# Kernel optimization log

Hardware: AMD Instinct MI355X
Metric: run time of the kernel (lower is better)

The kernel has to match this reference:

```python
import jax, jax.numpy as jnp
import numpy as np

DECAY = 0.7      # membrane decay
THETA = 1.0      # spike threshold
K_WINNERS = 5
GAIN_UP = 1.5
GAIN_DOWN = 0.6

SEQ_LEN = 8192
VOCAB = 128000


def setup_inputs() -> dict:
    key = jax.random.key(0)
    token_seq = jax.random.randint(key, (SEQ_LEN,), 0, VOCAB)  # int token ids
    v0 = jnp.zeros((VOCAB,), jnp.float32)  # initial membrane potentials
    return {"token_seq": token_seq, "v0": v0, "vocab_size": VOCAB}


def reference(token_seq, v0, vocab_size):
    spikes0 = jnp.zeros((vocab_size,), jnp.float32)

    def lif_step(state, token_id):
        v, spikes = state
        t = jnp.clip(token_id, 0, vocab_size - 1).astype(jnp.int32)
        v_new = DECAY * v[t] + 1.0                      # gather + decay + input current
        spiked = v_new >= THETA
        v = v.at[t].set(jnp.where(spiked, v_new - THETA, v_new))  # reset-by-subtraction
        spikes = spikes.at[t].add(spiked.astype(jnp.float32))
        return (v, spikes), None

    (v_final, spikes_final), _ = jax.lax.scan(lif_step, (v0, spikes0), token_seq)

    k = min(K_WINNERS, int(vocab_size))
    _, top_idx = jax.lax.top_k(v_final, k)
    winners = jnp.zeros((vocab_size,), jnp.float32).at[top_idx].set(1.0)
    gains = jnp.where(winners > 0, GAIN_UP,
                      jnp.where(spikes_final > 0, GAIN_DOWN, 1.0))
    return gains
```

## Files before the change

kernel.cpp:

```cpp
#include <hip/hip_runtime.h>
#include <float.h>
#include <limits.h>

#define DECAY 0.7f
#define THETA 1.0f
#define KWIN 5
#define GAIN_UP 1.5f
#define GAIN_DOWN 0.6f

__global__ void zero_counts(int* __restrict__ counts, int n) {
    int i = (blockIdx.x * blockDim.x + threadIdx.x) * 4;
    if (i + 3 < n) {
        *(int4*)(counts + i) = make_int4(0, 0, 0, 0);
    } else {
        for (int j = i; j < n; ++j) counts[j] = 0;
    }
}

__global__ void hist_kernel(const int* __restrict__ tok, int n, int vocab,
                            int* __restrict__ counts) {
    int i = (blockIdx.x * blockDim.x + threadIdx.x) * 4;
    if (i + 3 < n) {
        int4 t4 = *(const int4*)(tok + i);
        int t;
        t = min(max(t4.x, 0), vocab - 1); atomicAdd(&counts[t], 1);
        t = min(max(t4.y, 0), vocab - 1); atomicAdd(&counts[t], 1);
        t = min(max(t4.z, 0), vocab - 1); atomicAdd(&counts[t], 1);
        t = min(max(t4.w, 0), vocab - 1); atomicAdd(&counts[t], 1);
    } else {
        for (int j = i; j < n; ++j) {
            int t = min(max(tok[j], 0), vocab - 1);
            atomicAdd(&counts[t], 1);
        }
    }
}

__device__ __forceinline__ void lif_replay(float v0, int n, float& v_out, int& spikes_out) {
    float v = v0;
    int s = 0;
    for (int i = 0; i < n; ++i) {
        float vn = __fadd_rn(__fmul_rn(DECAY, v), 1.0f);
        if (vn >= THETA) { v = __fsub_rn(vn, THETA); ++s; }
        else             { v = vn; }
    }
    v_out = v;
    spikes_out = s;
}

__device__ __forceinline__ void better(float& bv, int& bi, float ov, int oi) {
    if (ov > bv || (ov == bv && oi < bi)) { bv = ov; bi = oi; }
}

__global__ void gains_top5(const int* __restrict__ counts,
                           const float* __restrict__ v0,
                           int vocab,
                           float* __restrict__ out,
                           float* __restrict__ cand_v,
                           int* __restrict__ cand_i) {
    int gid  = blockIdx.x * blockDim.x + threadIdx.x;
    int wave = gid >> 6;
    int lane = gid & 63;
    int base = wave * 256;

    float lv[4];
    int   li[4];
    #pragma unroll
    for (int k = 0; k < 4; ++k) {
        int idx = base + k * 64 + lane;
        float vf = -FLT_MAX;
        int   id = -1;
        if (idx < vocab) {
            int c = counts[idx];
            int s;
            lif_replay(v0[idx], c, vf, s);
            out[idx] = (s > 0) ? GAIN_DOWN : 1.0f;
            id = idx;
        }
        lv[k] = vf;
        li[k] = id;
    }

    #pragma unroll
    for (int r = 0; r < KWIN; ++r) {
        float bv = -FLT_MAX;
        int   bi = INT_MAX;
        #pragma unroll
        for (int k = 0; k < 4; ++k) {
            if (li[k] >= 0) better(bv, bi, lv[k], li[k]);
        }
        #pragma unroll
        for (int off = 32; off > 0; off >>= 1) {
            float ov = __shfl_xor(bv, off, 64);
            int   oi = __shfl_xor(bi, off, 64);
            better(bv, bi, ov, oi);
        }
        if (lane == 0) {
            cand_v[wave * KWIN + r] = bv;
            cand_i[wave * KWIN + r] = bi;
        }
        #pragma unroll
        for (int k = 0; k < 4; ++k) {
            if (li[k] == bi) li[k] = -1;
        }
    }
}

#define MAXC 8

__global__ void merge_top5(const float* __restrict__ cand_v,
                           const int* __restrict__ cand_i,
                           int n_cand,
                           float* __restrict__ out) {
    __shared__ unsigned long long swk[4];

    const int tid  = threadIdx.x;
    const int wave = tid >> 6;
    const int lane = tid & 63;

    unsigned long long k0 = 0ULL, k1 = 0ULL, k2 = 0ULL, k3 = 0ULL;
    unsigned long long k4 = 0ULL, k5 = 0ULL, k6 = 0ULL, k7 = 0ULL;
    #pragma unroll
    for (int s = 0; s < MAXC; ++s) {
        int j = s * 256 + tid;
        unsigned long long key = 0ULL;
        if (j < n_cand) {
            int ci = cand_i[j];
            if (ci >= 0 && ci != INT_MAX) {
                unsigned b  = __float_as_uint(cand_v[j]);
                unsigned sv = (b & 0x80000000u) ? ~b : (b | 0x80000000u);
                key = ((unsigned long long)sv << 32) | (unsigned)(~(unsigned)ci);
            }
        }
        if (s == 0) k0 = key; else if (s == 1) k1 = key;
        else if (s == 2) k2 = key; else if (s == 3) k3 = key;
        else if (s == 4) k4 = key; else if (s == 5) k5 = key;
        else if (s == 6) k6 = key; else k7 = key;
    }

    unsigned long long thresh = ~0ULL;
    for (int r = 0; r < KWIN; ++r) {
        unsigned long long best = 0ULL;
        if (k0 < thresh && k0 > best) best = k0;
        if (k1 < thresh && k1 > best) best = k1;
        if (k2 < thresh && k2 > best) best = k2;
        if (k3 < thresh && k3 > best) best = k3;
        if (k4 < thresh && k4 > best) best = k4;
        if (k5 < thresh && k5 > best) best = k5;
        if (k6 < thresh && k6 > best) best = k6;
        if (k7 < thresh && k7 > best) best = k7;

        #pragma unroll
        for (int off = 32; off > 0; off >>= 1) {
            unsigned hi = (unsigned)(best >> 32);
            unsigned lo = (unsigned)(best & 0xFFFFFFFFu);
            unsigned ohi = __shfl_xor(hi, off, 64);
            unsigned olo = __shfl_xor(lo, off, 64);
            unsigned long long ok = ((unsigned long long)ohi << 32) | olo;
            if (ok > best) best = ok;
        }
        if (lane == 0) swk[wave] = best;
        __syncthreads();

        unsigned long long bb = swk[0];
        if (swk[1] > bb) bb = swk[1];
        if (swk[2] > bb) bb = swk[2];
        if (swk[3] > bb) bb = swk[3];
        __syncthreads();

        if (tid == 0 && bb != 0ULL) {
            unsigned inv = (unsigned)(bb & 0xFFFFFFFFu);
            int idx = (int)(~inv);
            out[idx] = GAIN_UP;
        }
        thresh = bb;
    }
}

extern "C" void kernel_launch(void* const* d_in, const int* in_sizes, int n_in,
                              void* d_out, int out_size, void* d_ws, size_t ws_size,
                              hipStream_t stream) {
    const int*   tok = (const int*)d_in[0];
    const float* v0  = (const float*)d_in[1];
    int n     = in_sizes[0];
    int vocab = in_sizes[1];
    float* out = (float*)d_out;

    int nwaves = (vocab + 255) / 256;
    int gblocks = (vocab + 1023) / 1024;

    int*   counts = (int*)d_ws;
    float* cand_v = (float*)((char*)d_ws + (size_t)vocab * sizeof(int));
    int*   cand_i = (int*)(cand_v + (size_t)nwaves * KWIN);

    zero_counts<<<(vocab / 4 + 255) / 256 + 1, 256, 0, stream>>>(counts, vocab);
    hist_kernel<<<(n / 4 + 255) / 256 + 1, 256, 0, stream>>>(tok, n, vocab, counts);
    gains_top5<<<gblocks, 256, 0, stream>>>(counts, v0, vocab, out, cand_v, cand_i);
    merge_top5<<<1, 256, 0, stream>>>(cand_v, cand_i, nwaves * KWIN, out);
}
```

Baseline: 74.96 us.

## Fuse histogram into per-slice LDS histogram inside the gains kernel

Removes the zero_counts and global-atomic histogram kernels. Each block now scans the whole token sequence and builds a shared-memory histogram only for its 1024-entry vocabulary slice, then runs the LIF replay and per-wave top-5 directly. This cuts two launches and the global counts array, at the cost of every one of the 125 blocks rereading all 8192 tokens (32 KB each, mostly from L2). The merge kernel's per-thread candidate slots grow from 8 to 10 to match the new wave count.

```diff
diff --git a/kernel.cpp b/kernel.cpp
--- a/kernel.cpp
+++ b/kernel.cpp
@@ -8,32 +8,8 @@
 #define GAIN_UP 1.5f
 #define GAIN_DOWN 0.6f
 
-__global__ void zero_counts(int* __restrict__ counts, int n) {
-    int i = (blockIdx.x * blockDim.x + threadIdx.x) * 4;
-    if (i + 3 < n) {
-        *(int4*)(counts + i) = make_int4(0, 0, 0, 0);
-    } else {
-        for (int j = i; j < n; ++j) counts[j] = 0;
-    }
-}
-
-__global__ void hist_kernel(const int* __restrict__ tok, int n, int vocab,
-                            int* __restrict__ counts) {
-    int i = (blockIdx.x * blockDim.x + threadIdx.x) * 4;
-    if (i + 3 < n) {
-        int4 t4 = *(const int4*)(tok + i);
-        int t;
-        t = min(max(t4.x, 0), vocab - 1); atomicAdd(&counts[t], 1);
-        t = min(max(t4.y, 0), vocab - 1); atomicAdd(&counts[t], 1);
-        t = min(max(t4.z, 0), vocab - 1); atomicAdd(&counts[t], 1);
-        t = min(max(t4.w, 0), vocab - 1); atomicAdd(&counts[t], 1);
-    } else {
-        for (int j = i; j < n; ++j) {
-            int t = min(max(tok[j], 0), vocab - 1);
-            atomicAdd(&counts[t], 1);
-        }
-    }
-}
+#define NT 256
+#define SLICE 1024
 
 __device__ __forceinline__ void lif_replay(float v0, int n, float& v_out, int& spikes_out) {
     float v = v0;
@@ -51,26 +27,53 @@
     if (ov > bv || (ov == bv && oi < bi)) { bv = ov; bi = oi; }
 }
 
-__global__ void gains_top5(const int* __restrict__ counts,
-                           const float* __restrict__ v0,
-                           int vocab,
-                           float* __restrict__ out,
-                           float* __restrict__ cand_v,
-                           int* __restrict__ cand_i) {
-    int gid  = blockIdx.x * blockDim.x + threadIdx.x;
-    int wave = gid >> 6;
-    int lane = gid & 63;
-    int base = wave * 256;
-
+__global__ void fused_local(const int* __restrict__ tok,
+                            const float* __restrict__ v0,
+                            int n, int vocab,
+                            float* __restrict__ out,
+                            float* __restrict__ cand_v,
+                            int* __restrict__ cand_i) {
+    __shared__ int hist[SLICE];
+
+    const int tid  = threadIdx.x;
+    const int bid  = blockIdx.x;
+    const int wave = tid >> 6;
+    const int lane = tid & 63;
+    const int sbase = bid * SLICE;
+
+    #pragma unroll
+    for (int k = 0; k < SLICE / NT; ++k) {
+        hist[k * NT + tid] = 0;
+    }
+    __syncthreads();
+
+    int nv4 = n & ~3;
+    for (int j = tid * 4; j < nv4; j += NT * 4) {
+        int4 t4 = *(const int4*)(tok + j);
+        int t; unsigned r;
+        t = min(max(t4.x, 0), vocab - 1); r = (unsigned)(t - sbase); if (r < SLICE) atomicAdd(&hist[r], 1);
+        t = min(max(t4.y, 0), vocab - 1); r = (unsigned)(t - sbase); if (r < SLICE) atomicAdd(&hist[r], 1);
+        t = min(max(t4.z, 0), vocab - 1); r = (unsigned)(t - sbase); if (r < SLICE) atomicAdd(&hist[r], 1);
+        t = min(max(t4.w, 0), vocab - 1); r = (unsigned)(t - sbase); if (r < SLICE) atomicAdd(&hist[r], 1);
+    }
+    for (int j = nv4 + tid; j < n; j += NT) {
+        int t = min(max(tok[j], 0), vocab - 1);
+        unsigned r = (unsigned)(t - sbase);
+        if (r < SLICE) atomicAdd(&hist[r], 1);
+    }
+    __syncthreads();
+
+    const int wbase = wave * 256;
     float lv[4];
     int   li[4];
     #pragma unroll
     for (int k = 0; k < 4; ++k) {
-        int idx = base + k * 64 + lane;
+        int off = wbase + k * 64 + lane;
+        int idx = sbase + off;
         float vf = -FLT_MAX;
         int   id = -1;
         if (idx < vocab) {
-            int c = counts[idx];
+            int c = hist[off];
             int s;
             lif_replay(v0[idx], c, vf, s);
             out[idx] = (s > 0) ? GAIN_DOWN : 1.0f;
@@ -80,6 +83,7 @@
         li[k] = id;
     }
 
+    const int gw = bid * (NT / 64) + wave;
     #pragma unroll
     for (int r = 0; r < KWIN; ++r) {
         float bv = -FLT_MAX;
@@ -95,8 +99,8 @@
             better(bv, bi, ov, oi);
         }
         if (lane == 0) {
-            cand_v[wave * KWIN + r] = bv;
-            cand_i[wave * KWIN + r] = bi;
+            cand_v[gw * KWIN + r] = bv;
+            cand_i[gw * KWIN + r] = bi;
         }
         #pragma unroll
         for (int k = 0; k < 4; ++k) {
@@ -105,7 +109,7 @@
     }
 }
 
-#define MAXC 8
+#define MAXC 10
 
 __global__ void merge_top5(const float* __restrict__ cand_v,
                            const int* __restrict__ cand_i,
@@ -117,8 +121,8 @@
     const int wave = tid >> 6;
     const int lane = tid & 63;
 
-    unsigned long long k0 = 0ULL, k1 = 0ULL, k2 = 0ULL, k3 = 0ULL;
-    unsigned long long k4 = 0ULL, k5 = 0ULL, k6 = 0ULL, k7 = 0ULL;
+    unsigned long long k0 = 0ULL, k1 = 0ULL, k2 = 0ULL, k3 = 0ULL, k4 = 0ULL;
+    unsigned long long k5 = 0ULL, k6 = 0ULL, k7 = 0ULL, k8 = 0ULL, k9 = 0ULL;
     #pragma unroll
     for (int s = 0; s < MAXC; ++s) {
         int j = s * 256 + tid;
@@ -134,7 +138,8 @@
         if (s == 0) k0 = key; else if (s == 1) k1 = key;
         else if (s == 2) k2 = key; else if (s == 3) k3 = key;
         else if (s == 4) k4 = key; else if (s == 5) k5 = key;
-        else if (s == 6) k6 = key; else k7 = key;
+        else if (s == 6) k6 = key; else if (s == 7) k7 = key;
+        else if (s == 8) k8 = key; else k9 = key;
     }
 
     unsigned long long thresh = ~0ULL;
@@ -148,6 +153,8 @@
         if (k5 < thresh && k5 > best) best = k5;
         if (k6 < thresh && k6 > best) best = k6;
         if (k7 < thresh && k7 > best) best = k7;
+        if (k8 < thresh && k8 > best) best = k8;
+        if (k9 < thresh && k9 > best) best = k9;
 
         #pragma unroll
         for (int off = 32; off > 0; off >>= 1) {
@@ -185,15 +192,12 @@
     int vocab = in_sizes[1];
     float* out = (float*)d_out;
 
-    int nwaves = (vocab + 255) / 256;
-    int gblocks = (vocab + 1023) / 1024;
-
-    int*   counts = (int*)d_ws;
-    float* cand_v = (float*)((char*)d_ws + (size_t)vocab * sizeof(int));
+    int nb     = (vocab + SLICE - 1) / SLICE;
+    int nwaves = nb * (NT / 64);
+
+    float* cand_v = (float*)d_ws;
     int*   cand_i = (int*)(cand_v + (size_t)nwaves * KWIN);
 
-    zero_counts<<<(vocab / 4 + 255) / 256 + 1, 256, 0, stream>>>(counts, vocab);
-    hist_kernel<<<(n / 4 + 255) / 256 + 1, 256, 0, stream>>>(tok, n, vocab, counts);
-    gains_top5<<<gblocks, 256, 0, stream>>>(counts, v0, vocab, out, cand_v, cand_i);
-    merge_top5<<<1, 256, 0, stream>>>(cand_v, cand_i, nwaves * KWIN, out);
-}
+    fused_local<<<nb, NT, 0, stream>>>(tok, v0, n, vocab, out, cand_v, cand_i);
+    merge_top5<<<1, NT, 0, stream>>>(cand_v, cand_i, nwaves * KWIN, out);
+}
```

New measurement: 74.24 us. No clear change (-1.0%).
